# Performance work log

Measured on AMD Instinct MI355X. Metric: run time of the kernel, lower is better.

## Reference

```python
import jax, jax.numpy as jnp
import numpy as np

N_NODES = 100000
N_EDGES = 1600000
D_IN = 128
D_HID = 128
D_OUT = 64


def setup_inputs() -> dict:
    key = jax.random.key(0)
    ks = jax.random.split(key, 7)
    x = jax.random.normal(ks[0], (N_NODES, D_IN), dtype=jnp.float32)
    edge_index = jax.random.randint(ks[1], (2, N_EDGES), 0, N_NODES, dtype=jnp.int64)
    s = 1.0 / np.sqrt(D_IN)
    Wl1 = jax.random.normal(ks[2], (D_IN, D_HID), dtype=jnp.float32) * s
    Wr1 = jax.random.normal(ks[3], (D_IN, D_HID), dtype=jnp.float32) * s
    b1 = jnp.zeros((D_HID,), dtype=jnp.float32)
    s2 = 1.0 / np.sqrt(D_HID)
    Wl2 = jax.random.normal(ks[4], (D_HID, D_OUT), dtype=jnp.float32) * s2
    Wr2 = jax.random.normal(ks[5], (D_HID, D_OUT), dtype=jnp.float32) * s2
    b2 = jnp.zeros((D_OUT,), dtype=jnp.float32)
    return {"x": x, "edge_index": edge_index, "Wl1": Wl1, "Wr1": Wr1, "b1": b1,
            "Wl2": Wl2, "Wr2": Wr2, "b2": b2}


def _sage_conv(x, src, dst, Wl, Wr, b, n_nodes):
    # PyG SAGEConv, aggr='mean': out = lin_l(mean_{j in N(i)} x_j) + lin_r(x_i)
    msg = x[src]                                              # [E, D] gather
    agg = jax.ops.segment_sum(msg, dst, num_segments=n_nodes) # [N, D] scatter-add
    cnt = jax.ops.segment_sum(jnp.ones((src.shape[0],), x.dtype), dst,
                              num_segments=n_nodes)           # [N] in-degree
    agg = agg / jnp.maximum(cnt, 1.0)[:, None]                # mean (0 for isolated)
    return agg @ Wl + x @ Wr + b


def reference(x, edge_index, Wl1, Wr1, b1, Wl2, Wr2, b2):
    src, dst = edge_index[0], edge_index[1]  # source_to_target flow
    n = x.shape[0]
    h = jax.nn.relu(_sage_conv(x, src, dst, Wl1, Wr1, b1, n))
    out = _sage_conv(h, src, dst, Wl2, Wr2, b2, n)
    return out
```

## Files before the change

### kernel.cpp

```cpp
#include <hip/hip_runtime.h>


constexpr int TPB = 256;
constexpr int CAP = 64;
constexpr int NBIN = 256;
constexpr int NBLKA = 512;

typedef __attribute__((ext_vector_type(8))) short bf16x8;
typedef __attribute__((ext_vector_type(4))) float f32x4;

static __device__ __forceinline__ unsigned short f2bf(float f) {
    unsigned int u = __float_as_uint(f);
    u += 0x7fffu + ((u >> 16) & 1u);
    return (unsigned short)(u >> 16);
}
static __device__ __forceinline__ float bfe2f(short s) {
    return __uint_as_float(((unsigned int)(unsigned short)s) << 16);
}


__global__ void binA_count(const int* __restrict__ dst, int* __restrict__ blockhist,
                           int E, int epb) {
    __shared__ int hist[NBIN];
    hist[threadIdx.x] = 0;
    __syncthreads();
    int e0 = blockIdx.x * epb, e1 = min(E, e0 + epb);
    for (int i = e0 + threadIdx.x; i < e1; i += TPB)
        atomicAdd(&hist[dst[i] >> 9], 1);
    __syncthreads();
    blockhist[threadIdx.x * NBLKA + blockIdx.x] = hist[threadIdx.x];
}

__global__ void binA_total(const int* __restrict__ blockhist, int* __restrict__ bintotal) {
    __shared__ int s[TPB];
    int b = blockIdx.x;
    int sum = 0;
    for (int i = threadIdx.x; i < NBLKA; i += TPB) sum += blockhist[b * NBLKA + i];
    s[threadIdx.x] = sum;
    __syncthreads();
    for (int o = 128; o > 0; o >>= 1) {
        if (threadIdx.x < o) s[threadIdx.x] += s[threadIdx.x + o];
        __syncthreads();
    }
    if (threadIdx.x == 0) bintotal[b] = s[0];
}

__global__ void binA_scan(const int* __restrict__ bintotal, int* __restrict__ binstart) {
    __shared__ int s[NBIN];
    int t = threadIdx.x;
    s[t] = bintotal[t];
    __syncthreads();
    for (int o = 1; o < NBIN; o <<= 1) {
        int v = (t >= o) ? s[t - o] : 0;
        __syncthreads();
        s[t] += v;
        __syncthreads();
    }
    binstart[t] = t ? s[t - 1] : 0;
    if (t == NBIN - 1) binstart[NBIN] = s[NBIN - 1];
}

__global__ void binA_boff(const int* __restrict__ blockhist, const int* __restrict__ binstart,
                          int* __restrict__ boff) {
    __shared__ int s[NBLKA];
    int b = blockIdx.x, t = threadIdx.x;
    s[t] = blockhist[b * NBLKA + t];
    __syncthreads();
    for (int o = 1; o < NBLKA; o <<= 1) {
        int v = (t >= o) ? s[t - o] : 0;
        __syncthreads();
        s[t] += v;
        __syncthreads();
    }
    int excl = t ? s[t - 1] : 0;
    boff[b * NBLKA + t] = binstart[b] + excl;
}

__global__ void binA_scatter(const int* __restrict__ src, const int* __restrict__ dst,
                             const int* __restrict__ boff, int2* __restrict__ sorted,
                             int E, int epb) {
    __shared__ int base[NBIN];
    __shared__ int lcur[NBIN];
    int t = threadIdx.x, blk = blockIdx.x;
    base[t] = boff[t * NBLKA + blk];
    lcur[t] = 0;
    __syncthreads();
    int e0 = blk * epb, e1 = min(E, e0 + epb);
    for (int i = e0 + t; i < e1; i += TPB) {
        int d = dst[i];
        int b = d >> 9;
        int p = base[b] + atomicAdd(&lcur[b], 1);
        sorted[p] = make_int2(src[i], d);
    }
}

__global__ void binB_build(const int2* __restrict__ sorted, const int* __restrict__ binstart,
                           int* __restrict__ cursor, int* __restrict__ nbrp, int N) {
    __shared__ int lcur[512];
    int t = threadIdx.x, b = blockIdx.x;
    lcur[t] = 0;
    lcur[t + 256] = 0;
    __syncthreads();
    int lo = binstart[b], hi = binstart[b + 1];
    int node0 = b << 9;
    for (int i = lo + t; i < hi; i += TPB) {
        int2 e = sorted[i];
        int p = atomicAdd(&lcur[e.y - node0], 1);
        if (p < CAP) nbrp[(size_t)e.y * CAP + p] = e.x;
    }
    __syncthreads();
    for (int k = t; k < 512; k += TPB) {
        int node = node0 + k;
        if (node < N) cursor[node] = lcur[k];
    }
}

__global__ void cast_bf16_kernel(const float* __restrict__ in, unsigned short* __restrict__ out,
                                 int n4) {
    int i = blockIdx.x * TPB + threadIdx.x;
    if (i < n4) {
        float4 v = ((const float4*)in)[i];
        ushort4 o;
        o.x = f2bf(v.x); o.y = f2bf(v.y); o.z = f2bf(v.z); o.w = f2bf(v.w);
        ((ushort4*)out)[i] = o;
    }
}

__global__ void weight_prep_kernel(const float* __restrict__ Wl1, const float* __restrict__ Wr1,
                                   const float* __restrict__ Wl2, const float* __restrict__ Wr2,
                                   unsigned short* __restrict__ Wt1,
                                   unsigned short* __restrict__ Wt2a,
                                   unsigned short* __restrict__ Wt2b) {
    int idx = blockIdx.x * TPB + threadIdx.x;
    if (idx < 128 * 256) {
        int co = idx & 127, k = idx >> 7;
        float v = (k < 128) ? Wl1[k * 128 + co] : Wr1[(k - 128) * 128 + co];
        Wt1[(size_t)co * 256 + k] = f2bf(v);
    } else if (idx < 128 * 256 + 64 * 128) {
        int j = idx - 128 * 256;
        int co = j & 63, k = j >> 6;
        Wt2a[(size_t)co * 128 + k] = f2bf(Wl2[k * 64 + co]);
    } else if (idx < 128 * 256 + 2 * 64 * 128) {
        int j = idx - 128 * 256 - 64 * 128;
        int co = j & 63, k = j >> 6;
        Wt2b[(size_t)co * 128 + k] = f2bf(Wr2[k * 64 + co]);
    }
}

template <int D, bool FINALADD>
__global__ __launch_bounds__(256) void gather_mean_kernel(
    const unsigned short* __restrict__ feat,
    const int* __restrict__ nbrp,
    const int* __restrict__ cursor,
    const float* __restrict__ ub,
    void* __restrict__ outv,
    int N) {
    constexpr int LPN = D / 8;
    int gid = blockIdx.x * TPB + threadIdx.x;
    int node = gid / LPN;
    if (node >= N) return;
    const int lane = threadIdx.x & 63;
    const int part = lane & (LPN - 1);
    const int base = lane & ~(LPN - 1);
    const unsigned short* fcol = feat + part * 8;

    const int* lst = nbrp + (size_t)node * CAP;
    int dtrue = cursor[node];
    int d = min(dtrue, CAP);
    int d32 = min(d, 32);

    int id0 = lst[part];
    int id1 = lst[LPN + part];
    int id2 = 0, id3 = 0;
    if (LPN == 8) {
        id2 = lst[2 * LPN + part];
        id3 = lst[3 * LPN + part];
    }

    float a0[8], a1[8], a2[8], a3[8];
#pragma unroll
    for (int i = 0; i < 8; i++) { a0[i] = 0.f; a1[i] = 0.f; a2[i] = 0.f; a3[i] = 0.f; }

    int j = 0;
    for (; j + 7 < d32; j += 8) {
        int k = j / LPN;
        if (LPN == 8) k = j >> 3;
        int sel = (k == 0) ? id0 : (k == 1) ? id1 : (k == 2) ? id2 : id3;
        int sl = base + (j & (LPN - 1));
        int s0 = __shfl(sel, sl + 0);
        int s1 = __shfl(sel, sl + 1);
        int s2 = __shfl(sel, sl + 2);
        int s3 = __shfl(sel, sl + 3);
        int s4 = __shfl(sel, sl + 4);
        int s5 = __shfl(sel, sl + 5);
        int s6 = __shfl(sel, sl + 6);
        int s7 = __shfl(sel, sl + 7);
        bf16x8 v0 = *(const bf16x8*)(fcol + (size_t)s0 * D);
        bf16x8 v1 = *(const bf16x8*)(fcol + (size_t)s1 * D);
        bf16x8 v2 = *(const bf16x8*)(fcol + (size_t)s2 * D);
        bf16x8 v3 = *(const bf16x8*)(fcol + (size_t)s3 * D);
        bf16x8 v4 = *(const bf16x8*)(fcol + (size_t)s4 * D);
        bf16x8 v5 = *(const bf16x8*)(fcol + (size_t)s5 * D);
        bf16x8 v6 = *(const bf16x8*)(fcol + (size_t)s6 * D);
        bf16x8 v7 = *(const bf16x8*)(fcol + (size_t)s7 * D);
#pragma unroll
        for (int i = 0; i < 8; i++) {
            a0[i] += bfe2f(v0[i]);
            a1[i] += bfe2f(v1[i]);
            a2[i] += bfe2f(v2[i]);
            a3[i] += bfe2f(v3[i]);
        }
#pragma unroll
        for (int i = 0; i < 8; i++) {
            a0[i] += bfe2f(v4[i]);
            a1[i] += bfe2f(v5[i]);
            a2[i] += bfe2f(v6[i]);
            a3[i] += bfe2f(v7[i]);
        }
    }
    for (; j < d32; j++) {
        int blk = j / LPN;
        int sel = (blk == 0) ? id0 : (blk == 1) ? id1 : (blk == 2) ? id2 : id3;
        int s0 = __shfl(sel, base + (j & (LPN - 1)));
        bf16x8 v0 = *(const bf16x8*)(fcol + (size_t)s0 * D);
#pragma unroll
        for (int i = 0; i < 8; i++) a0[i] += bfe2f(v0[i]);
    }
    for (; j < d; j++) {
        int s0 = lst[j];
        bf16x8 v0 = *(const bf16x8*)(fcol + (size_t)s0 * D);
#pragma unroll
        for (int i = 0; i < 8; i++) a0[i] += bfe2f(v0[i]);
    }

    float sc = 1.0f / (float)max(dtrue, 1);
    float r[8];
#pragma unroll
    for (int i = 0; i < 8; i++) r[i] = (a0[i] + a1[i] + a2[i] + a3[i]) * sc;

    if (FINALADD) {
        const float* up = ub + (size_t)node * D + part * 8;
        float* op = (float*)outv + (size_t)node * D + part * 8;
        float4 u0 = *(const float4*)(up);
        float4 u1 = *(const float4*)(up + 4);
        float4 o0 = make_float4(r[0] + u0.x, r[1] + u0.y, r[2] + u0.z, r[3] + u0.w);
        float4 o1 = make_float4(r[4] + u1.x, r[5] + u1.y, r[6] + u1.z, r[7] + u1.w);
        *(float4*)(op) = o0;
        *(float4*)(op + 4) = o1;
    } else {
        bf16x8 st;
#pragma unroll
        for (int i = 0; i < 8; i++) st[i] = (short)f2bf(r[i]);
        *(bf16x8*)((unsigned short*)outv + (size_t)node * D + part * 8) = st;
    }
}

__global__ __launch_bounds__(256) void sage1_mfma_kernel(
    const unsigned short* __restrict__ A1,
    const unsigned short* __restrict__ A2,
    const unsigned short* __restrict__ Wt,
    const float* __restrict__ bias,
    unsigned short* __restrict__ outb,
    int N, int ntiles) {
    constexpr int K = 256, KS = 8;

    const int tid = threadIdx.x;
    const int lane = tid & 63;
    const int wave = tid >> 6;
    const int lrow = lane & 15;
    const int kb = (lane >> 4) * 8;
    const int colgrp = wave & 1;
    const int mslot = wave >> 1;
    const int colbase = colgrp * 64;

    bf16x8 B[4][KS];
#pragma unroll
    for (int t = 0; t < 4; t++)
#pragma unroll
        for (int ks = 0; ks < KS; ks++)
            B[t][ks] = *(const bf16x8*)(Wt + (size_t)(colbase + t * 16 + lrow) * K + ks * 32 + kb);

    for (int tile = blockIdx.x * 2 + mslot; tile < ntiles; tile += gridDim.x * 2) {
        const int m0 = tile * 16;
        const int arow = min(m0 + lrow, N - 1);

        bf16x8 a[KS];
#pragma unroll
        for (int ks = 0; ks < KS; ks++) {
            if (ks >= 4)
                a[ks] = *(const bf16x8*)(A2 + (size_t)arow * 128 + (ks - 4) * 32 + kb);
            else
                a[ks] = *(const bf16x8*)(A1 + (size_t)arow * 128 + ks * 32 + kb);
        }

        f32x4 acc[4];
#pragma unroll
        for (int t = 0; t < 4; t++) acc[t] = (f32x4){0.f, 0.f, 0.f, 0.f};
#pragma unroll
        for (int ks = 0; ks < KS; ks++)
#pragma unroll
            for (int t = 0; t < 4; t++)
                acc[t] = __builtin_amdgcn_mfma_f32_16x16x32_bf16(a[ks], B[t][ks], acc[t], 0, 0, 0);

        const int mb = m0 + (lane >> 4) * 4;
#pragma unroll
        for (int t = 0; t < 4; t++) {
            const int col = colbase + t * 16 + lrow;
            const float bv = bias[col];
#pragma unroll
            for (int r = 0; r < 4; r++) {
                const int m = mb + r;
                if (m < N) {
                    float v = fmaxf(acc[t][r] + bv, 0.f);
                    outb[(size_t)m * 128 + col] = f2bf(v);
                }
            }
        }
    }
}

__global__ __launch_bounds__(256) void gemm64_dual_kernel(
    const unsigned short* __restrict__ h,
    const unsigned short* __restrict__ Wta,
    const unsigned short* __restrict__ Wtb,
    const float* __restrict__ bias,
    unsigned short* __restrict__ tb,
    float* __restrict__ ub,
    int N, int ntiles) {
    constexpr int K = 128, KS = 4;

    const int tid = threadIdx.x;
    const int lane = tid & 63;
    const int wave = tid >> 6;
    const int lrow = lane & 15;
    const int kb = (lane >> 4) * 8;

    bf16x8 Ba[4][KS], Bb[4][KS];
#pragma unroll
    for (int t = 0; t < 4; t++)
#pragma unroll
        for (int ks = 0; ks < KS; ks++) {
            Ba[t][ks] = *(const bf16x8*)(Wta + (size_t)(t * 16 + lrow) * K + ks * 32 + kb);
            Bb[t][ks] = *(const bf16x8*)(Wtb + (size_t)(t * 16 + lrow) * K + ks * 32 + kb);
        }

    for (int tile = blockIdx.x * 4 + wave; tile < ntiles; tile += gridDim.x * 4) {
        const int m0 = tile * 16;
        const int arow = min(m0 + lrow, N - 1);

        bf16x8 a[KS];
#pragma unroll
        for (int ks = 0; ks < KS; ks++)
            a[ks] = *(const bf16x8*)(h + (size_t)arow * 128 + ks * 32 + kb);

        f32x4 acct[4], accu[4];
#pragma unroll
        for (int t = 0; t < 4; t++) {
            acct[t] = (f32x4){0.f, 0.f, 0.f, 0.f};
            accu[t] = (f32x4){0.f, 0.f, 0.f, 0.f};
        }
#pragma unroll
        for (int ks = 0; ks < KS; ks++)
#pragma unroll
            for (int t = 0; t < 4; t++) {
                acct[t] = __builtin_amdgcn_mfma_f32_16x16x32_bf16(a[ks], Ba[t][ks], acct[t], 0, 0, 0);
                accu[t] = __builtin_amdgcn_mfma_f32_16x16x32_bf16(a[ks], Bb[t][ks], accu[t], 0, 0, 0);
            }

        const int mb = m0 + (lane >> 4) * 4;
#pragma unroll
        for (int t = 0; t < 4; t++) {
            const int col = t * 16 + lrow;
            const float bv = bias[col];
#pragma unroll
            for (int r = 0; r < 4; r++) {
                const int m = mb + r;
                if (m < N) {
                    tb[(size_t)m * 64 + col] = f2bf(acct[t][r]);
                    ub[(size_t)m * 64 + col] = accu[t][r] + bv;
                }
            }
        }
    }
}

extern "C" void kernel_launch(void* const* d_in, const int* in_sizes, int n_in,
                              void* d_out, int out_size, void* d_ws, size_t ws_size,
                              hipStream_t stream) {
    const float* x   = (const float*)d_in[0];
    const int* ei    = (const int*)d_in[1];
    const float* Wl1 = (const float*)d_in[2];
    const float* Wr1 = (const float*)d_in[3];
    const float* b1  = (const float*)d_in[4];
    const float* Wl2 = (const float*)d_in[5];
    const float* Wr2 = (const float*)d_in[6];
    const float* b2  = (const float*)d_in[7];
    float* out = (float*)d_out;

    const int N = in_sizes[0] / 128;
    const int E = in_sizes[1] / 2;
    const int* src = ei;
    const int* dst = ei + E;

    const int epb = (E + NBLKA - 1) / NBLKA;
    const int ntiles = (N + 15) / 16;
    const int nNodeBins = (N + 511) >> 9;

    unsigned short* xb = (unsigned short*)d_out;
    float* ub          = (float*)d_out;

    unsigned short* h    = (unsigned short*)d_ws;
    unsigned short* aggb = h + (size_t)N * 128;
    int2* sorted         = (int2*)aggb;
    unsigned short* tb   = aggb + (size_t)N * 128;
    unsigned short* Wt1  = tb + (size_t)N * 64;
    unsigned short* Wt2a = Wt1 + 128 * 256;
    unsigned short* Wt2b = Wt2a + 64 * 128;
    int* cursor    = (int*)(Wt2b + 64 * 128);
    int* nbrp      = cursor + N;
    int* blockhist = nbrp + (size_t)N * CAP;
    int* bintotal  = blockhist + NBIN * NBLKA;
    int* binstart  = bintotal + NBIN;
    int* boff      = binstart + (NBIN + 1);

    weight_prep_kernel<<<(128 * 256 + 2 * 64 * 128 + TPB - 1) / TPB, TPB, 0, stream>>>(
        Wl1, Wr1, Wl2, Wr2, Wt1, Wt2a, Wt2b);
    binA_count<<<NBLKA, TPB, 0, stream>>>(dst, blockhist, E, epb);
    binA_total<<<NBIN, TPB, 0, stream>>>(blockhist, bintotal);
    binA_scan<<<1, NBIN, 0, stream>>>(bintotal, binstart);
    binA_boff<<<NBIN, NBLKA, 0, stream>>>(blockhist, binstart, boff);
    binA_scatter<<<NBLKA, TPB, 0, stream>>>(src, dst, boff, sorted, E, epb);
    binB_build<<<nNodeBins, TPB, 0, stream>>>(sorted, binstart, cursor, nbrp, N);

    cast_bf16_kernel<<<((N * 128 / 4) + TPB - 1) / TPB, TPB, 0, stream>>>(x, xb, N * 128 / 4);
    gather_mean_kernel<128, false><<<(N * 16 + TPB - 1) / TPB, TPB, 0, stream>>>(
        xb, nbrp, cursor, nullptr, aggb, N);
    sage1_mfma_kernel<<<512, 256, 0, stream>>>(aggb, xb, Wt1, b1, h, N, ntiles);

    gemm64_dual_kernel<<<512, 256, 0, stream>>>(h, Wt2a, Wt2b, b2, tb, ub, N, ntiles);
    gather_mean_kernel<64, true><<<(N * 8 + TPB - 1) / TPB, TPB, 0, stream>>>(
        tb, nbrp, cursor, ub, out, N);
}
```

Baseline: 206.8 us.

## Sort nodes by degree within bins and tighten gather unroll for balance

binB_build now counting-sorts each 512-node bin by in-degree and writes a permutation (pnode). The gather kernels then process nodes in that order, so wavefronts hold nodes of similar degree and waste fewer lanes waiting on long neighbour lists. The main gather loop drops from 8 to 4 neighbours per step and uses a masked 3-way tail instead of a scalar remainder loop. The cost is an extra indirection per node, a serial per-block scan, and scattered rather than contiguous output writes.

```diff
diff --git a/kernel.cpp b/kernel.cpp
--- a/kernel.cpp
+++ b/kernel.cpp
@@ -95,24 +95,38 @@
 }
 
 __global__ void binB_build(const int2* __restrict__ sorted, const int* __restrict__ binstart,
-                           int* __restrict__ cursor, int* __restrict__ nbrp, int N) {
+                           int* __restrict__ cursor, int* __restrict__ nbrp,
+                           int* __restrict__ pnode, int N) {
     __shared__ int lcur[512];
+    __shared__ int hist[CAP + 1];
     int t = threadIdx.x, b = blockIdx.x;
     lcur[t] = 0;
     lcur[t + 256] = 0;
+    if (t <= CAP) hist[t] = 0;
     __syncthreads();
     int lo = binstart[b], hi = binstart[b + 1];
     int node0 = b << 9;
+    int cnt = min(512, N - node0);
     for (int i = lo + t; i < hi; i += TPB) {
         int2 e = sorted[i];
         int p = atomicAdd(&lcur[e.y - node0], 1);
         if (p < CAP) nbrp[(size_t)e.y * CAP + p] = e.x;
     }
     __syncthreads();
-    for (int k = t; k < 512; k += TPB) {
+    for (int k = t; k < cnt; k += TPB) atomicAdd(&hist[min(lcur[k], CAP)], 1);
+    __syncthreads();
+    if (t == 0) {
+        int run = 0;
+        for (int q = 0; q <= CAP; q++) { int c = hist[q]; hist[q] = run; run += c; }
+    }
+    __syncthreads();
+    for (int k = t; k < cnt; k += TPB) {
         int node = node0 + k;
-        if (node < N) cursor[node] = lcur[k];
-    }
+        cursor[node] = lcur[k];
+        int r = atomicAdd(&hist[min(lcur[k], CAP)], 1);
+        pnode[(b << 9) + r] = node;
+    }
+    for (int k = cnt + t; k < 512; k += TPB) pnode[(b << 9) + k] = -1;
 }
 
 __global__ void cast_bf16_kernel(const float* __restrict__ in, unsigned short* __restrict__ out,
@@ -152,13 +166,16 @@
     const unsigned short* __restrict__ feat,
     const int* __restrict__ nbrp,
     const int* __restrict__ cursor,
+    const int* __restrict__ pnode,
     const float* __restrict__ ub,
     void* __restrict__ outv,
-    int N) {
+    int nslot) {
     constexpr int LPN = D / 8;
     int gid = blockIdx.x * TPB + threadIdx.x;
-    int node = gid / LPN;
-    if (node >= N) return;
+    int slot = gid / LPN;
+    if (slot >= nslot) return;
+    int node = pnode[slot];
+    if (node < 0) return;
     const int lane = threadIdx.x & 63;
     const int part = lane & (LPN - 1);
     const int base = lane & ~(LPN - 1);
@@ -182,27 +199,19 @@
     for (int i = 0; i < 8; i++) { a0[i] = 0.f; a1[i] = 0.f; a2[i] = 0.f; a3[i] = 0.f; }
 
     int j = 0;
-    for (; j + 7 < d32; j += 8) {
-        int k = j / LPN;
-        if (LPN == 8) k = j >> 3;
-        int sel = (k == 0) ? id0 : (k == 1) ? id1 : (k == 2) ? id2 : id3;
+    int full = d32 & ~3;
+    for (; j < full; j += 4) {
+        int blk = (LPN == 8) ? (j >> 3) : (j >> 4);
+        int sel = (blk == 0) ? id0 : (blk == 1) ? id1 : (blk == 2) ? id2 : id3;
         int sl = base + (j & (LPN - 1));
         int s0 = __shfl(sel, sl + 0);
         int s1 = __shfl(sel, sl + 1);
         int s2 = __shfl(sel, sl + 2);
         int s3 = __shfl(sel, sl + 3);
-        int s4 = __shfl(sel, sl + 4);
-        int s5 = __shfl(sel, sl + 5);
-        int s6 = __shfl(sel, sl + 6);
-        int s7 = __shfl(sel, sl + 7);
         bf16x8 v0 = *(const bf16x8*)(fcol + (size_t)s0 * D);
         bf16x8 v1 = *(const bf16x8*)(fcol + (size_t)s1 * D);
         bf16x8 v2 = *(const bf16x8*)(fcol + (size_t)s2 * D);
         bf16x8 v3 = *(const bf16x8*)(fcol + (size_t)s3 * D);
-        bf16x8 v4 = *(const bf16x8*)(fcol + (size_t)s4 * D);
-        bf16x8 v5 = *(const bf16x8*)(fcol + (size_t)s5 * D);
-        bf16x8 v6 = *(const bf16x8*)(fcol + (size_t)s6 * D);
-        bf16x8 v7 = *(const bf16x8*)(fcol + (size_t)s7 * D);
 #pragma unroll
         for (int i = 0; i < 8; i++) {
             a0[i] += bfe2f(v0[i]);
@@ -210,21 +219,28 @@
             a2[i] += bfe2f(v2[i]);
             a3[i] += bfe2f(v3[i]);
         }
+    }
+    if (j < d32) {
+        int blk = (LPN == 8) ? (j >> 3) : (j >> 4);
+        int sel = (blk == 0) ? id0 : (blk == 1) ? id1 : (blk == 2) ? id2 : id3;
+        int sl = base + (j & (LPN - 1));
+        int s0 = __shfl(sel, sl + 0);
+        int s1 = __shfl(sel, sl + 1);
+        int s2 = __shfl(sel, sl + 2);
+        bool m1 = (j + 1 < d32), m2 = (j + 2 < d32);
+        s1 = m1 ? s1 : s0;
+        s2 = m2 ? s2 : s0;
+        float f1 = m1 ? 1.f : 0.f, f2 = m2 ? 1.f : 0.f;
+        bf16x8 v0 = *(const bf16x8*)(fcol + (size_t)s0 * D);
+        bf16x8 v1 = *(const bf16x8*)(fcol + (size_t)s1 * D);
+        bf16x8 v2 = *(const bf16x8*)(fcol + (size_t)s2 * D);
 #pragma unroll
         for (int i = 0; i < 8; i++) {
-            a0[i] += bfe2f(v4[i]);
-            a1[i] += bfe2f(v5[i]);
-            a2[i] += bfe2f(v6[i]);
-            a3[i] += bfe2f(v7[i]);
-        }
-    }
-    for (; j < d32; j++) {
-        int blk = j / LPN;
-        int sel = (blk == 0) ? id0 : (blk == 1) ? id1 : (blk == 2) ? id2 : id3;
-        int s0 = __shfl(sel, base + (j & (LPN - 1)));
-        bf16x8 v0 = *(const bf16x8*)(fcol + (size_t)s0 * D);
-#pragma unroll
-        for (int i = 0; i < 8; i++) a0[i] += bfe2f(v0[i]);
+            a0[i] += bfe2f(v0[i]);
+            a1[i] = fmaf(f1, bfe2f(v1[i]), a1[i]);
+            a2[i] = fmaf(f2, bfe2f(v2[i]), a2[i]);
+        }
+        j = d32;
     }
     for (; j < d; j++) {
         int s0 = lst[j];
@@ -405,6 +421,7 @@
     const int epb = (E + NBLKA - 1) / NBLKA;
     const int ntiles = (N + 15) / 16;
     const int nNodeBins = (N + 511) >> 9;
+    const int nslot = nNodeBins << 9;
 
     unsigned short* xb = (unsigned short*)d_out;
     float* ub          = (float*)d_out;
@@ -422,6 +439,7 @@
     int* bintotal  = blockhist + NBIN * NBLKA;
     int* binstart  = bintotal + NBIN;
     int* boff      = binstart + (NBIN + 1);
+    int* pnode     = boff + NBIN * NBLKA;
 
     weight_prep_kernel<<<(128 * 256 + 2 * 64 * 128 + TPB - 1) / TPB, TPB, 0, stream>>>(
         Wl1, Wr1, Wl2, Wr2, Wt1, Wt2a, Wt2b);
@@ -430,14 +448,14 @@
     binA_scan<<<1, NBIN, 0, stream>>>(bintotal, binstart);
     binA_boff<<<NBIN, NBLKA, 0, stream>>>(blockhist, binstart, boff);
     binA_scatter<<<NBLKA, TPB, 0, stream>>>(src, dst, boff, sorted, E, epb);
-    binB_build<<<nNodeBins, TPB, 0, stream>>>(sorted, binstart, cursor, nbrp, N);
+    binB_build<<<nNodeBins, TPB, 0, stream>>>(sorted, binstart, cursor, nbrp, pnode, N);
 
     cast_bf16_kernel<<<((N * 128 / 4) + TPB - 1) / TPB, TPB, 0, stream>>>(x, xb, N * 128 / 4);
-    gather_mean_kernel<128, false><<<(N * 16 + TPB - 1) / TPB, TPB, 0, stream>>>(
-        xb, nbrp, cursor, nullptr, aggb, N);
+    gather_mean_kernel<128, false><<<(nslot * 16 + TPB - 1) / TPB, TPB, 0, stream>>>(
+        xb, nbrp, cursor, pnode, nullptr, aggb, nslot);
     sage1_mfma_kernel<<<512, 256, 0, stream>>>(aggb, xb, Wt1, b1, h, N, ntiles);
 
     gemm64_dual_kernel<<<512, 256, 0, stream>>>(h, Wt2a, Wt2b, b2, tb, ub, N, ntiles);
-    gather_mean_kernel<64, true><<<(N * 8 + TPB - 1) / TPB, TPB, 0, stream>>>(
-        tb, nbrp, cursor, ub, out, N);
-}
+    gather_mean_kernel<64, true><<<(nslot * 8 + TPB - 1) / TPB, TPB, 0, stream>>>(
+        tb, nbrp, cursor, pnode, ub, out, nslot);
+}
```

Result: slower. 213.2 us (+3.1%).
